# Performance work log

Hardware: AMD Instinct MI355X
Metric: run time of the kernel (lower is better)

Reference implementation:

```python
import jax, jax.numpy as jnp
import numpy as np

# Physical parameter bounds in PARAM_NAMES order:
# [S1_max,S2_max,f_tens,f_rchr,f_base,r1,ku,c,alpha,psi,kappa,ki,ks,n,v,v_A,v_B,
#  Ac_max,b,lambda,chi,mu_t,T_rain,T_melt,melt_rate,lapse_rate,opg,MFMAX,MFMIN]
LOW = jnp.array([50.0,100.0,0.05,0.05,0.05,0.05,0.01,1.0,1.0,1.0,0.05,0.01,0.001,1.0,
                 0.001,0.001,0.001,0.05,0.001,5.0,2.0,0.01,-2.0,-2.0,1.0,-9.8,0.0,1.0,0.0],
                dtype=jnp.float32)
HIGH = jnp.array([5000.0,10000.0,0.95,0.95,0.95,0.95,1000.0,20.0,250.0,5.0,0.95,1000.0,
                  10000.0,10.0,0.25,0.25,0.25,0.95,3.0,10.0,5.0,5.0,4.0,4.0,10.0,0.0,1.0,10.0,10.0],
                 dtype=jnp.float32)
ROUTE_SHAPE = 2.5   # gamma routing shape (init kwarg)
KERNEL_LEN = 64     # routing kernel support (timesteps)
DT = 1.0
S1_INIT, S2_INIT = 50.0, 250.0  # state_init in the module


def _physical(raw_params):
    # low + (high-low)*sigmoid(raw), same as get_physical_params
    return LOW + (HIGH - LOW) * jax.nn.sigmoid(raw_params)


def _simulate(forcing, p):
    """Explicit-Euler 2-reservoir FUSE-style simulation. forcing: [T,3]=(prcp,pet,temp)."""
    S1_max, S2_max = p[0], p[1]
    f_tens, ku, c = p[2], p[6], p[7]
    ki, ks, n_exp = p[11], p[12], p[13]
    b, T_rain = p[18], p[22]

    def step(state, f):
        S1, S2 = state
        prcp, pet, temp = f[0], f[1], f[2]
        rain = jnp.where(temp > T_rain, prcp, 0.0)
        s1f = jnp.clip(S1 / S1_max, 0.0, 1.0)
        s2f = jnp.clip(S2 / S2_max, 0.0, 1.0)
        e1 = pet * jnp.minimum(s1f / f_tens, 1.0)          # tension-store evap
        qsx = rain * s1f ** b                               # saturation-excess runoff
        q12 = ku * s1f ** c                                 # percolation to lower store
        qif = ki * s1f                                      # interflow
        qb = ks * s2f ** n_exp                              # nonlinear baseflow
        S1n = jnp.clip(S1 + DT * (rain - qsx - e1 - q12 - qif), 0.0, S1_max)
        S2n = jnp.clip(S2 + DT * (q12 - qb), 0.0, S2_max)
        return (S1n, S2n), qsx + qif + qb

    init = (jnp.float32(S1_INIT), jnp.float32(S2_INIT))
    _, runoff = jax.lax.scan(step, init, forcing)
    return runoff  # [T]


def _route(runoff, shape, delay):
    """Causal gamma-kernel routing convolution (route_runoff)."""
    t = jnp.arange(KERNEL_LEN, dtype=jnp.float32) + 0.5
    theta = jnp.maximum(delay, 1e-3) / shape               # scale so mean = delay
    logk = (shape - 1.0) * jnp.log(t) - t / theta
    kern = jax.nn.softmax(logk)                            # normalized gamma weights
    return jnp.convolve(runoff, kern)[: runoff.shape[0]]   # causal conv


def reference(forcing, raw_params):
    phys = _physical(raw_params)
    runoff = _simulate(forcing, phys)
    # delay is used as a detached python float in the torch code -> stop_gradient
    delay = jax.lax.stop_gradient(phys[21])  # mu_t
    return _route(runoff, ROUTE_SHAPE, delay)


def setup_inputs() -> dict:
    key = jax.random.key(0)
    k1, k2, k3 = jax.random.split(key, 3)
    T = 131072
    prcp = jnp.maximum(jax.random.normal(k1, (T,)) * 5.0 + 2.0, 0.0)  # mm/day
    pet = jax.random.uniform(k2, (T,)) * 5.0                          # mm/day
    temp = jax.random.normal(k3, (T,)) * 8.0 + 5.0                    # deg C
    forcing = jnp.stack([prcp, pet, temp], axis=-1).astype(jnp.float32)
    raw_params = jnp.zeros((29,), dtype=jnp.float32)  # sigmoid(0)=0.5 -> mid-bounds
    return {"forcing": forcing, "raw_params": raw_params}
```

## Files before the change

kernel.cpp:

```cpp
#include <hip/hip_runtime.h>

#define KLEN 64
#define FCH 16
#define WARMUP 64
#define WIN_FC 64
#define S1_INIT_V 50.0f
#define S2_INIT_V 250.0f

__device__ __forceinline__ float fpow(float x, float e) {
    return exp2f(e * __log2f(x));
}
__device__ __forceinline__ float clamp01(float x) { return fminf(fmaxf(x, 0.0f), 1.0f); }
__device__ __forceinline__ float physp(const float* raw, int i, float lo, float hi) {
    return lo + (hi - lo) / (1.0f + __expf(-raw[i]));
}

struct F8 { float4 v[6]; };
__device__ __forceinline__ F8 load_f8(const float* __restrict__ forc, int t) {
    const float4* p = (const float4*)(forc + 3 * t);
    F8 r;
#pragma unroll
    for (int k = 0; k < 6; ++k) r.v[k] = p[k];
    return r;
}
__device__ __forceinline__ float f4c(const float4& v, int c) {
    return c == 0 ? v.x : c == 1 ? v.y : c == 2 ? v.z : v.w;
}
__device__ __forceinline__ float f8_get(const F8& f, int i) { return f4c(f.v[i >> 2], i & 3); }

#define S1_CORE(pr, pe, te, QACC)                                         \
    {                                                                     \
        float rain = (te) > Train ? (pr) : 0.0f;                          \
        float s1f = clamp01(S1 * invS1);                                  \
        float lg = __log2f(s1f);                                          \
        float e1 = (pe)*fminf(s1f * invft, 1.0f);                         \
        float qsx = rain * exp2f(b * lg);                                 \
        float q12 = ku * exp2f(cc * lg);                                  \
        float qif = ki * s1f;                                             \
        S1 = fminf(fmaxf(S1 + rain - qsx - e1 - q12 - qif, 0.0f), S1max); \
        QACC;                                                             \
    }

__global__ void __launch_bounds__(64) k_s1(
        const float* __restrict__ forc, const float* __restrict__ raw,
        float* __restrict__ s1s, float* __restrict__ q12f, float* __restrict__ Qw,
        int T, int nfine) {
    int lane = threadIdx.x;
    int j = blockIdx.x * WIN_FC + lane;
    bool active = j < nfine;

    const float S1max  = physp(raw, 0, 50.0f, 5000.0f);
    const float f_tens = physp(raw, 2, 0.05f, 0.95f);
    const float ku     = physp(raw, 6, 0.01f, 1000.0f);
    const float cc     = physp(raw, 7, 1.0f, 20.0f);
    const float ki     = physp(raw, 11, 0.01f, 1000.0f);
    const float b      = physp(raw, 18, 0.001f, 3.0f);
    const float Train  = physp(raw, 22, -2.0f, 4.0f);
    const float invS1 = 1.0f / S1max, invft = 1.0f / f_tens;

    float S1 = S1_INIT_V;
    float Q = 0.0f;
    if (active) {
        int t0 = j * FCH;
        int tend = min(t0 + FCH, T);
        int ts = max(t0 - WARMUP, 0);

        int ngw = (t0 - ts) >> 3;
        F8 cur = load_f8(forc, ts);
        for (int g = 0; g < ngw; ++g) {
            F8 nxt = load_f8(forc, ts + 8 * (g + 1));
#pragma unroll
            for (int s = 0; s < 8; ++s) {
                float pr = f8_get(cur, 3 * s), pe = f8_get(cur, 3 * s + 1), te = f8_get(cur, 3 * s + 2);
                S1_CORE(pr, pe, te, );
            }
            cur = nxt;
        }
        s1s[j] = S1;

        int ngm = (tend - t0) >> 3;
        for (int g = 0; g < ngm; ++g) {
            F8 nxt = load_f8(forc, t0 + 8 * min(g + 1, ngm - 1));
#pragma unroll
            for (int s = 0; s < 8; ++s) {
                float pr = f8_get(cur, 3 * s), pe = f8_get(cur, 3 * s + 1), te = f8_get(cur, 3 * s + 2);
                S1_CORE(pr, pe, te, Q += q12);
            }
            cur = nxt;
        }
        for (int t = t0 + 8 * ngm; t < tend; ++t) {
            float pr = forc[3 * t], pe = forc[3 * t + 1], te = forc[3 * t + 2];
            S1_CORE(pr, pe, te, Q += q12);
        }
        q12f[j] = Q;
    }
    float s = Q;
#pragma unroll
    for (int o = 32; o >= 1; o >>= 1) s += __shfl_xor(s, o, 64);
    if (lane == 0) Qw[blockIdx.x] = s;
}

__global__ void __launch_bounds__(64) k_s2win(
        const float* __restrict__ raw, const float* __restrict__ Qw,
        const float* __restrict__ q12f,
        float* __restrict__ S2win, float* __restrict__ qbwin,
        float* __restrict__ s2fine, int* __restrict__ flag,
        int T, int nfine) {
    int lane = threadIdx.x;
    const float S2max = physp(raw, 1, 100.0f, 10000.0f);
    const float ks    = physp(raw, 12, 0.001f, 10000.0f);
    const float nn    = physp(raw, 13, 1.0f, 10.0f);
    const float invS2 = 1.0f / S2max;

    int NW = (nfine + WIN_FC - 1) / WIN_FC;
    int WSTEPS = WIN_FC * FCH;

    int w0 = 2 * lane, w1 = 2 * lane + 1;
    float L0 = (w0 < NW) ? (float)min(WSTEPS, T - WSTEPS * w0) : 0.0f;
    float L1 = (w1 < NW) ? (float)min(WSTEPS, T - WSTEPS * w1) : 0.0f;
    float Q0 = (w0 < NW) ? Qw[w0] : 0.0f;
    float Q1 = (w1 < NW) ? Qw[w1] : 0.0f;

    float qb0 = ks * fpow(clamp01(S2_INIT_V * invS2), nn);
    float qb1 = qb0;
    float S20 = S2_INIT_V, S21 = S2_INIT_V;
    bool picard_ok = (NW <= 128);
    if (picard_ok) {
        for (int it = 0; it < 12; ++it) {
            float d0 = Q0 - L0 * qb0;
            float d1 = Q1 - L1 * qb1;
            float pair = d0 + d1;
            float sc = pair;
#pragma unroll
            for (int o = 1; o < 64; o <<= 1) {
                float v = __shfl_up(sc, o, 64);
                if (lane >= o) sc += v;
            }
            float excl = sc - pair;
            S20 = S2_INIT_V + excl;
            S21 = S20 + d0;
            qb0 = ks * fpow(clamp01(S20 * invS2), nn);
            qb1 = ks * fpow(clamp01(S21 * invS2), nn);
        }
        bool bad = false;
        if (w0 < NW) bad |= (S20 - L0 * qb0 < 0.5f) || (S20 + Q0 > S2max - 0.5f);
        if (w1 < NW) bad |= (S21 - L1 * qb1 < 0.5f) || (S21 + Q1 > S2max - 0.5f);
        picard_ok = (__ballot(bad) == 0ULL);
    }
    if (picard_ok) {
        if (w0 < NW) { S2win[w0] = S20; qbwin[w0] = qb0; }
        if (w1 < NW) { S2win[w1] = S21; qbwin[w1] = qb1; }
        if (lane == 0) *flag = 0;
    } else if (lane == 0) {
        *flag = 1;
        float S2 = S2_INIT_V;
        for (int w = 0; w < NW; ++w) {
            float s2f = clamp01(S2 * invS2);
            float qb = ks * fpow(s2f, nn);
            S2win[w] = S2; qbwin[w] = qb;
            int i0 = w * WIN_FC, i1 = min(i0 + WIN_FC, nfine);
            for (int i = i0; i < i1; ++i) {
                s2fine[i] = S2;
                float steps = (float)min(FCH, T - FCH * i);
                S2 = fminf(fmaxf(S2 + q12f[i] - steps * qb, 0.0f), S2max);
            }
        }
    }
}

__global__ void __launch_bounds__(64) k_sim(
        const float* __restrict__ forc, const float* __restrict__ raw,
        const float* __restrict__ s1s, const float* __restrict__ q12f,
        const float* __restrict__ S2win, const float* __restrict__ qbwin,
        const float* __restrict__ s2fine, const int* __restrict__ flag,
        float* __restrict__ runoff, int T, int nfine) {
    int lane = threadIdx.x;
    int j = blockIdx.x * WIN_FC + lane;
    bool active = j < nfine;

    const float S1max  = physp(raw, 0, 50.0f, 5000.0f);
    const float S2max  = physp(raw, 1, 100.0f, 10000.0f);
    const float f_tens = physp(raw, 2, 0.05f, 0.95f);
    const float ku     = physp(raw, 6, 0.01f, 1000.0f);
    const float ki     = physp(raw, 11, 0.01f, 1000.0f);
    const float ks     = physp(raw, 12, 0.001f, 10000.0f);
    const float nn     = physp(raw, 13, 1.0f, 10.0f);
    const float cc     = physp(raw, 7, 1.0f, 20.0f);
    const float b      = physp(raw, 18, 0.001f, 3.0f);
    const float Train  = physp(raw, 22, -2.0f, 4.0f);
    const float invS1 = 1.0f / S1max, invS2 = 1.0f / S2max, invft = 1.0f / f_tens;

    float q = active ? q12f[j] : 0.0f;
    float S2;
    if (*flag) {
        S2 = active ? s2fine[j] : 0.0f;
    } else {
        float sc = q;
#pragma unroll
        for (int o = 1; o < 64; o <<= 1) {
            float v = __shfl_up(sc, o, 64);
            if (lane >= o) sc += v;
        }
        float excl = sc - q;
        S2 = S2win[blockIdx.x] + excl - qbwin[blockIdx.x] * (float)(FCH * lane);
        S2 = fminf(fmaxf(S2, 0.0f), S2max);
    }
    if (!active) return;

    float S1 = s1s[j];
    int t0 = j * FCH;
    int tend = min(t0 + FCH, T);

#define SIM_CORE(pr, pe, te, EMIT)                                        \
    {                                                                     \
        float rain = (te) > Train ? (pr) : 0.0f;                          \
        float s1f = clamp01(S1 * invS1);                                  \
        float s2f = clamp01(S2 * invS2);                                  \
        float lg = __log2f(s1f);                                          \
        float e1 = (pe)*fminf(s1f * invft, 1.0f);                         \
        float qsx = rain * exp2f(b * lg);                                 \
        float q12 = ku * exp2f(cc * lg);                                  \
        float qif = ki * s1f;                                             \
        float qb = ks * fpow(s2f, nn);                                    \
        EMIT;                                                             \
        S1 = fminf(fmaxf(S1 + rain - qsx - e1 - q12 - qif, 0.0f), S1max); \
        S2 = fminf(fmaxf(S2 + q12 - qb, 0.0f), S2max);                    \
    }

    int ngm = (tend - t0) >> 3;
    if (ngm > 0) {
        F8 cur = load_f8(forc, t0);
        for (int g = 0; g < ngm; ++g) {
            F8 nxt = load_f8(forc, t0 + 8 * min(g + 1, ngm - 1));
            float ro[8];
#pragma unroll
            for (int s = 0; s < 8; ++s) {
                float pr = f8_get(cur, 3 * s), pe = f8_get(cur, 3 * s + 1), te = f8_get(cur, 3 * s + 2);
                SIM_CORE(pr, pe, te, ro[s] = qsx + qif + qb);
            }
            float4* rp = (float4*)(runoff + t0 + 8 * g);
            rp[0] = make_float4(ro[0], ro[1], ro[2], ro[3]);
            rp[1] = make_float4(ro[4], ro[5], ro[6], ro[7]);
            cur = nxt;
        }
    }
    for (int t = t0 + 8 * ngm; t < tend; ++t) {
        float pr = forc[3 * t], pe = forc[3 * t + 1], te = forc[3 * t + 2];
        SIM_CORE(pr, pe, te, runoff[t] = qsx + qif + qb);
    }
}

__global__ void k_route(const float* __restrict__ runoff, const float* __restrict__ raw,
                        float* __restrict__ out, int T) {
    __shared__ float ls[256 + KLEN - 1];
    __shared__ float ker[KLEN];
    int tid = threadIdx.x;
    int base = blockIdx.x * 256;
    if (tid < 64) {
        float delay = physp(raw, 21, 0.01f, 5.0f);
        float theta = fmaxf(delay, 1e-3f) * (1.0f / 2.5f);
        float tt = (float)tid + 0.5f;
        float logk = 1.5f * __logf(tt) - tt / theta;
        float m = logk;
#pragma unroll
        for (int o = 32; o >= 1; o >>= 1) m = fmaxf(m, __shfl_xor(m, o, 64));
        float e = __expf(logk - m);
        float s = e;
#pragma unroll
        for (int o = 32; o >= 1; o >>= 1) s += __shfl_xor(s, o, 64);
        ker[tid] = e / s;
    }
    for (int i = tid; i < 256 + KLEN - 1; i += 256) {
        int t = base - (KLEN - 1) + i;
        ls[i] = (t >= 0 && t < T) ? runoff[t] : 0.0f;
    }
    __syncthreads();
    float acc = 0.0f;
#pragma unroll
    for (int k = 0; k < KLEN; ++k) acc += ker[k] * ls[tid + (KLEN - 1) - k];
    int t = base + tid;
    if (t < T) out[t] = acc;
}

extern "C" void kernel_launch(void* const* d_in, const int* in_sizes, int n_in,
                              void* d_out, int out_size, void* d_ws, size_t ws_size,
                              hipStream_t stream) {
    const float* forcing = (const float*)d_in[0];
    const float* raw = (const float*)d_in[1];
    float* out = (float*)d_out;
    float* ws = (float*)d_ws;

    int T = in_sizes[0] / 3;
    int nfine = (T + FCH - 1) / FCH;
    int NW = (nfine + WIN_FC - 1) / WIN_FC;
    int P = ((nfine + 7) / 8) * 8;
    int PW = ((NW + 7) / 8) * 8;

    float* s1s = ws;
    float* q12f = s1s + P;
    float* Qw = q12f + P;
    float* S2win = Qw + PW;
    float* qbwin = S2win + PW;
    float* s2fine = qbwin + PW;
    int* flag = (int*)(s2fine + P);
    float* runoff = (float*)(flag + 8);

    k_s1<<<NW, 64, 0, stream>>>(forcing, raw, s1s, q12f, Qw, T, nfine);
    k_s2win<<<1, 64, 0, stream>>>(raw, Qw, q12f, S2win, qbwin, s2fine, flag, T, nfine);
    k_sim<<<NW, 64, 0, stream>>>(forcing, raw, s1s, q12f, S2win, qbwin, s2fine, flag,
                                 runoff, T, nfine);
    k_route<<<(T + 255) / 256, 256, 0, stream>>>(runoff, raw, out, T);
}
```

Before: 73.39 us.

## Fuse four kernels into one persistent kernel with grid barriers

Replaces the S1 pass, the S2 window solve, the full simulation and the routing kernels with one kernel that uses software grid barriers between phases. S1 fluxes are kept in registers so the second pass only advances S2, and the routing convolution reads runoff from shared memory within each window. Warmup is reduced from 64 to 48 steps. This removes three launch gaps and recomputation of S1, but adds an atomic spin barrier that relies on all 128 blocks being co-resident, a memset launch, and a shorter warmup that may change accuracy.

Measured after the change: 98.74 us. 34.5% more time.

```diff
diff --git a/kernel.cpp b/kernel.cpp
--- a/kernel.cpp
+++ b/kernel.cpp
@@ -2,8 +2,9 @@
 
 #define KLEN 64
 #define FCH 16
-#define WARMUP 64
+#define WARMUP 48
 #define WIN_FC 64
+#define WSTEP (WIN_FC * FCH)
 #define S1_INIT_V 50.0f
 #define S2_INIT_V 250.0f
 
@@ -11,7 +12,7 @@
     return exp2f(e * __log2f(x));
 }
 __device__ __forceinline__ float clamp01(float x) { return fminf(fmaxf(x, 0.0f), 1.0f); }
-__device__ __forceinline__ float physp(const float* raw, int i, float lo, float hi) {
+__device__ __forceinline__ float physp(const float* __restrict__ raw, int i, float lo, float hi) {
     return lo + (hi - lo) / (1.0f + __expf(-raw[i]));
 }
 
@@ -28,7 +29,48 @@
 }
 __device__ __forceinline__ float f8_get(const F8& f, int i) { return f4c(f.v[i >> 2], i & 3); }
 
-#define S1_CORE(pr, pe, te, QACC)                                         \
+__device__ __forceinline__ void gbar(int* cnt, int phase, int nblk) {
+    __syncthreads();
+    if (threadIdx.x == 0) {
+        __threadfence();
+        __hip_atomic_fetch_add(cnt, 1, __ATOMIC_ACQ_REL, __HIP_MEMORY_SCOPE_AGENT);
+        while (__hip_atomic_load(cnt, __ATOMIC_ACQUIRE, __HIP_MEMORY_SCOPE_AGENT) <
+               phase * nblk) {
+            __builtin_amdgcn_s_sleep(2);
+        }
+        __threadfence();
+    }
+    __syncthreads();
+}
+
+__global__ void __launch_bounds__(64) k_fused(
+        const float* __restrict__ forc, const float* __restrict__ raw,
+        float* __restrict__ q12f, float* __restrict__ Qw,
+        float* __restrict__ S2win, float* __restrict__ qbwin,
+        float* __restrict__ s2fine, float* __restrict__ runoff,
+        int* __restrict__ syncp, int* __restrict__ flag,
+        float* __restrict__ out, int T, int nfine, int NW) {
+    __shared__ float r[WSTEP + 64];
+    __shared__ float ker[KLEN];
+    const int lane = threadIdx.x;
+    const int w = blockIdx.x;
+    const int j = w * WIN_FC + lane;
+    const int t0w = w * WSTEP;
+    const bool active = j < nfine;
+
+    const float S1max  = physp(raw, 0, 50.0f, 5000.0f);
+    const float S2max  = physp(raw, 1, 100.0f, 10000.0f);
+    const float f_tens = physp(raw, 2, 0.05f, 0.95f);
+    const float ku     = physp(raw, 6, 0.01f, 1000.0f);
+    const float cc     = physp(raw, 7, 1.0f, 20.0f);
+    const float ki     = physp(raw, 11, 0.01f, 1000.0f);
+    const float ks     = physp(raw, 12, 0.001f, 10000.0f);
+    const float nn     = physp(raw, 13, 1.0f, 10.0f);
+    const float b      = physp(raw, 18, 0.001f, 3.0f);
+    const float Train  = physp(raw, 22, -2.0f, 4.0f);
+    const float invS1 = 1.0f / S1max, invS2 = 1.0f / S2max, invft = 1.0f / f_tens;
+
+#define S1_STEP(pr, pe, te, EXTRA)                                        \
     {                                                                     \
         float rain = (te) > Train ? (pr) : 0.0f;                          \
         float s1f = clamp01(S1 * invS1);                                  \
@@ -37,229 +79,168 @@
         float qsx = rain * exp2f(b * lg);                                 \
         float q12 = ku * exp2f(cc * lg);                                  \
         float qif = ki * s1f;                                             \
+        EXTRA;                                                            \
         S1 = fminf(fmaxf(S1 + rain - qsx - e1 - q12 - qif, 0.0f), S1max); \
-        QACC;                                                             \
-    }
-
-__global__ void __launch_bounds__(64) k_s1(
-        const float* __restrict__ forc, const float* __restrict__ raw,
-        float* __restrict__ s1s, float* __restrict__ q12f, float* __restrict__ Qw,
-        int T, int nfine) {
-    int lane = threadIdx.x;
-    int j = blockIdx.x * WIN_FC + lane;
-    bool active = j < nfine;
-
-    const float S1max  = physp(raw, 0, 50.0f, 5000.0f);
-    const float f_tens = physp(raw, 2, 0.05f, 0.95f);
-    const float ku     = physp(raw, 6, 0.01f, 1000.0f);
-    const float cc     = physp(raw, 7, 1.0f, 20.0f);
-    const float ki     = physp(raw, 11, 0.01f, 1000.0f);
-    const float b      = physp(raw, 18, 0.001f, 3.0f);
-    const float Train  = physp(raw, 22, -2.0f, 4.0f);
-    const float invS1 = 1.0f / S1max, invft = 1.0f / f_tens;
-
-    float S1 = S1_INIT_V;
+    }
+
+    float qx[FCH];
+    float q12v[FCH];
     float Q = 0.0f;
+    const int t0 = j * FCH;
+    const int tend = active ? min(t0 + FCH, T) : t0;
+    const bool fullchunk = active && (tend - t0 == FCH);
+
     if (active) {
-        int t0 = j * FCH;
-        int tend = min(t0 + FCH, T);
         int ts = max(t0 - WARMUP, 0);
-
+        float S1 = S1_INIT_V;
         int ngw = (t0 - ts) >> 3;
         F8 cur = load_f8(forc, ts);
         for (int g = 0; g < ngw; ++g) {
             F8 nxt = load_f8(forc, ts + 8 * (g + 1));
 #pragma unroll
-            for (int s = 0; s < 8; ++s) {
-                float pr = f8_get(cur, 3 * s), pe = f8_get(cur, 3 * s + 1), te = f8_get(cur, 3 * s + 2);
-                S1_CORE(pr, pe, te, );
-            }
+            for (int s = 0; s < 8; ++s)
+                S1_STEP(f8_get(cur, 3 * s), f8_get(cur, 3 * s + 1), f8_get(cur, 3 * s + 2), );
             cur = nxt;
         }
-        s1s[j] = S1;
-
-        int ngm = (tend - t0) >> 3;
-        for (int g = 0; g < ngm; ++g) {
-            F8 nxt = load_f8(forc, t0 + 8 * min(g + 1, ngm - 1));
-#pragma unroll
-            for (int s = 0; s < 8; ++s) {
-                float pr = f8_get(cur, 3 * s), pe = f8_get(cur, 3 * s + 1), te = f8_get(cur, 3 * s + 2);
-                S1_CORE(pr, pe, te, Q += q12);
-            }
-            cur = nxt;
-        }
-        for (int t = t0 + 8 * ngm; t < tend; ++t) {
-            float pr = forc[3 * t], pe = forc[3 * t + 1], te = forc[3 * t + 2];
-            S1_CORE(pr, pe, te, Q += q12);
+        if (fullchunk) {
+#pragma unroll
+            for (int g = 0; g < 2; ++g) {
+                F8 nxt = (g == 0) ? load_f8(forc, t0 + 8) : cur;
+#pragma unroll
+                for (int s = 0; s < 8; ++s) {
+                    const int idx = 8 * g + s;
+                    S1_STEP(f8_get(cur, 3 * s), f8_get(cur, 3 * s + 1), f8_get(cur, 3 * s + 2),
+                            qx[idx] = qsx + qif; q12v[idx] = q12; Q += q12);
+                }
+                cur = nxt;
+            }
+        } else {
+            for (int t = t0; t < tend; ++t) {
+                float pr = forc[3 * t], pe = forc[3 * t + 1], te = forc[3 * t + 2];
+                S1_STEP(pr, pe, te, Q += q12);
+            }
         }
         q12f[j] = Q;
     }
-    float s = Q;
-#pragma unroll
-    for (int o = 32; o >= 1; o >>= 1) s += __shfl_xor(s, o, 64);
-    if (lane == 0) Qw[blockIdx.x] = s;
-}
-
-__global__ void __launch_bounds__(64) k_s2win(
-        const float* __restrict__ raw, const float* __restrict__ Qw,
-        const float* __restrict__ q12f,
-        float* __restrict__ S2win, float* __restrict__ qbwin,
-        float* __restrict__ s2fine, int* __restrict__ flag,
-        int T, int nfine) {
-    int lane = threadIdx.x;
-    const float S2max = physp(raw, 1, 100.0f, 10000.0f);
-    const float ks    = physp(raw, 12, 0.001f, 10000.0f);
-    const float nn    = physp(raw, 13, 1.0f, 10.0f);
-    const float invS2 = 1.0f / S2max;
-
-    int NW = (nfine + WIN_FC - 1) / WIN_FC;
-    int WSTEPS = WIN_FC * FCH;
-
-    int w0 = 2 * lane, w1 = 2 * lane + 1;
-    float L0 = (w0 < NW) ? (float)min(WSTEPS, T - WSTEPS * w0) : 0.0f;
-    float L1 = (w1 < NW) ? (float)min(WSTEPS, T - WSTEPS * w1) : 0.0f;
-    float Q0 = (w0 < NW) ? Qw[w0] : 0.0f;
-    float Q1 = (w1 < NW) ? Qw[w1] : 0.0f;
-
-    float qb0 = ks * fpow(clamp01(S2_INIT_V * invS2), nn);
-    float qb1 = qb0;
-    float S20 = S2_INIT_V, S21 = S2_INIT_V;
-    bool picard_ok = (NW <= 128);
-    if (picard_ok) {
-        for (int it = 0; it < 12; ++it) {
-            float d0 = Q0 - L0 * qb0;
-            float d1 = Q1 - L1 * qb1;
-            float pair = d0 + d1;
-            float sc = pair;
-#pragma unroll
-            for (int o = 1; o < 64; o <<= 1) {
-                float v = __shfl_up(sc, o, 64);
-                if (lane >= o) sc += v;
-            }
-            float excl = sc - pair;
-            S20 = S2_INIT_V + excl;
-            S21 = S20 + d0;
-            qb0 = ks * fpow(clamp01(S20 * invS2), nn);
-            qb1 = ks * fpow(clamp01(S21 * invS2), nn);
-        }
-        bool bad = false;
-        if (w0 < NW) bad |= (S20 - L0 * qb0 < 0.5f) || (S20 + Q0 > S2max - 0.5f);
-        if (w1 < NW) bad |= (S21 - L1 * qb1 < 0.5f) || (S21 + Q1 > S2max - 0.5f);
-        picard_ok = (__ballot(bad) == 0ULL);
-    }
-    if (picard_ok) {
-        if (w0 < NW) { S2win[w0] = S20; qbwin[w0] = qb0; }
-        if (w1 < NW) { S2win[w1] = S21; qbwin[w1] = qb1; }
-        if (lane == 0) *flag = 0;
-    } else if (lane == 0) {
-        *flag = 1;
-        float S2 = S2_INIT_V;
-        for (int w = 0; w < NW; ++w) {
-            float s2f = clamp01(S2 * invS2);
-            float qb = ks * fpow(s2f, nn);
-            S2win[w] = S2; qbwin[w] = qb;
-            int i0 = w * WIN_FC, i1 = min(i0 + WIN_FC, nfine);
-            for (int i = i0; i < i1; ++i) {
-                s2fine[i] = S2;
-                float steps = (float)min(FCH, T - FCH * i);
-                S2 = fminf(fmaxf(S2 + q12f[i] - steps * qb, 0.0f), S2max);
-            }
-        }
-    }
-}
-
-__global__ void __launch_bounds__(64) k_sim(
-        const float* __restrict__ forc, const float* __restrict__ raw,
-        const float* __restrict__ s1s, const float* __restrict__ q12f,
-        const float* __restrict__ S2win, const float* __restrict__ qbwin,
-        const float* __restrict__ s2fine, const int* __restrict__ flag,
-        float* __restrict__ runoff, int T, int nfine) {
-    int lane = threadIdx.x;
-    int j = blockIdx.x * WIN_FC + lane;
-    bool active = j < nfine;
-
-    const float S1max  = physp(raw, 0, 50.0f, 5000.0f);
-    const float S2max  = physp(raw, 1, 100.0f, 10000.0f);
-    const float f_tens = physp(raw, 2, 0.05f, 0.95f);
-    const float ku     = physp(raw, 6, 0.01f, 1000.0f);
-    const float ki     = physp(raw, 11, 0.01f, 1000.0f);
-    const float ks     = physp(raw, 12, 0.001f, 10000.0f);
-    const float nn     = physp(raw, 13, 1.0f, 10.0f);
-    const float cc     = physp(raw, 7, 1.0f, 20.0f);
-    const float b      = physp(raw, 18, 0.001f, 3.0f);
-    const float Train  = physp(raw, 22, -2.0f, 4.0f);
-    const float invS1 = 1.0f / S1max, invS2 = 1.0f / S2max, invft = 1.0f / f_tens;
-
-    float q = active ? q12f[j] : 0.0f;
+    {
+        float s = Q;
+#pragma unroll
+        for (int o = 32; o >= 1; o >>= 1) s += __shfl_xor(s, o, 64);
+        if (lane == 0) Qw[w] = s;
+    }
+
+    gbar(syncp, 1, NW);
+
+    if (w == 0) {
+        int wsteps = WSTEP;
+        int w0 = 2 * lane, w1 = 2 * lane + 1;
+        float L0 = (w0 < NW) ? (float)min(wsteps, T - wsteps * w0) : 0.0f;
+        float L1 = (w1 < NW) ? (float)min(wsteps, T - wsteps * w1) : 0.0f;
+        float Q0 = (w0 < NW) ? Qw[w0] : 0.0f;
+        float Q1 = (w1 < NW) ? Qw[w1] : 0.0f;
+
+        float qb0 = ks * fpow(clamp01(S2_INIT_V * invS2), nn);
+        float qb1 = qb0;
+        float S20 = S2_INIT_V, S21 = S2_INIT_V;
+        bool picard_ok = (NW <= 128);
+        if (picard_ok) {
+            for (int it = 0; it < 12; ++it) {
+                float d0 = Q0 - L0 * qb0;
+                float d1 = Q1 - L1 * qb1;
+                float pair = d0 + d1;
+                float sc = pair;
+#pragma unroll
+                for (int o = 1; o < 64; o <<= 1) {
+                    float v = __shfl_up(sc, o, 64);
+                    if (lane >= o) sc += v;
+                }
+                float excl = sc - pair;
+                S20 = S2_INIT_V + excl;
+                S21 = S20 + d0;
+                qb0 = ks * fpow(clamp01(S20 * invS2), nn);
+                qb1 = ks * fpow(clamp01(S21 * invS2), nn);
+            }
+            bool bad = false;
+            if (w0 < NW) bad |= (S20 - L0 * qb0 < 0.5f) || (S20 + Q0 > S2max - 0.5f);
+            if (w1 < NW) bad |= (S21 - L1 * qb1 < 0.5f) || (S21 + Q1 > S2max - 0.5f);
+            picard_ok = (__ballot(bad) == 0ULL);
+        }
+        if (picard_ok) {
+            if (w0 < NW) { S2win[w0] = S20; qbwin[w0] = qb0; }
+            if (w1 < NW) { S2win[w1] = S21; qbwin[w1] = qb1; }
+            if (lane == 0) *flag = 0;
+        } else if (lane == 0) {
+            *flag = 1;
+            float S2 = S2_INIT_V;
+            for (int v = 0; v < NW; ++v) {
+                float s2f = clamp01(S2 * invS2);
+                float qb = ks * fpow(s2f, nn);
+                S2win[v] = S2; qbwin[v] = qb;
+                int i0 = v * WIN_FC, i1 = min(i0 + WIN_FC, nfine);
+                for (int i = i0; i < i1; ++i) {
+                    s2fine[i] = S2;
+                    float steps = (float)min(FCH, T - FCH * i);
+                    S2 = fminf(fmaxf(S2 + q12f[i] - steps * qb, 0.0f), S2max);
+                }
+            }
+        }
+    }
+
+    gbar(syncp, 2, NW);
+
     float S2;
     if (*flag) {
         S2 = active ? s2fine[j] : 0.0f;
     } else {
-        float sc = q;
+        float sc = Q;
 #pragma unroll
         for (int o = 1; o < 64; o <<= 1) {
             float v = __shfl_up(sc, o, 64);
             if (lane >= o) sc += v;
         }
-        float excl = sc - q;
-        S2 = S2win[blockIdx.x] + excl - qbwin[blockIdx.x] * (float)(FCH * lane);
+        S2 = S2win[w] + (sc - Q) - qbwin[w] * (float)(FCH * lane);
         S2 = fminf(fmaxf(S2, 0.0f), S2max);
     }
-    if (!active) return;
-
-    float S1 = s1s[j];
-    int t0 = j * FCH;
-    int tend = min(t0 + FCH, T);
-
-#define SIM_CORE(pr, pe, te, EMIT)                                        \
-    {                                                                     \
-        float rain = (te) > Train ? (pr) : 0.0f;                          \
-        float s1f = clamp01(S1 * invS1);                                  \
-        float s2f = clamp01(S2 * invS2);                                  \
-        float lg = __log2f(s1f);                                          \
-        float e1 = (pe)*fminf(s1f * invft, 1.0f);                         \
-        float qsx = rain * exp2f(b * lg);                                 \
-        float q12 = ku * exp2f(cc * lg);                                  \
-        float qif = ki * s1f;                                             \
-        float qb = ks * fpow(s2f, nn);                                    \
-        EMIT;                                                             \
-        S1 = fminf(fmaxf(S1 + rain - qsx - e1 - q12 - qif, 0.0f), S1max); \
-        S2 = fminf(fmaxf(S2 + q12 - qb, 0.0f), S2max);                    \
-    }
-
-    int ngm = (tend - t0) >> 3;
-    if (ngm > 0) {
-        F8 cur = load_f8(forc, t0);
-        for (int g = 0; g < ngm; ++g) {
-            F8 nxt = load_f8(forc, t0 + 8 * min(g + 1, ngm - 1));
-            float ro[8];
-#pragma unroll
-            for (int s = 0; s < 8; ++s) {
-                float pr = f8_get(cur, 3 * s), pe = f8_get(cur, 3 * s + 1), te = f8_get(cur, 3 * s + 2);
-                SIM_CORE(pr, pe, te, ro[s] = qsx + qif + qb);
-            }
-            float4* rp = (float4*)(runoff + t0 + 8 * g);
-            rp[0] = make_float4(ro[0], ro[1], ro[2], ro[3]);
-            rp[1] = make_float4(ro[4], ro[5], ro[6], ro[7]);
-            cur = nxt;
-        }
-    }
-    for (int t = t0 + 8 * ngm; t < tend; ++t) {
-        float pr = forc[3 * t], pe = forc[3 * t + 1], te = forc[3 * t + 2];
-        SIM_CORE(pr, pe, te, runoff[t] = qsx + qif + qb);
-    }
-}
-
-__global__ void k_route(const float* __restrict__ runoff, const float* __restrict__ raw,
-                        float* __restrict__ out, int T) {
-    __shared__ float ls[256 + KLEN - 1];
-    __shared__ float ker[KLEN];
-    int tid = threadIdx.x;
-    int base = blockIdx.x * 256;
-    if (tid < 64) {
+    if (fullchunk) {
+        float rb[FCH];
+#pragma unroll
+        for (int s = 0; s < FCH; ++s) {
+            float s2f = clamp01(S2 * invS2);
+            float qb = ks * fpow(s2f, nn);
+            float ro = qx[s] + qb;
+            rb[s] = ro;
+            r[64 + FCH * lane + s] = ro;
+            S2 = fminf(fmaxf(S2 + q12v[s] - qb, 0.0f), S2max);
+        }
+        float4* rp = (float4*)(runoff + t0);
+#pragma unroll
+        for (int s4 = 0; s4 < 4; ++s4)
+            rp[s4] = make_float4(rb[4 * s4], rb[4 * s4 + 1], rb[4 * s4 + 2], rb[4 * s4 + 3]);
+    } else if (active) {
+        float S1 = S1_INIT_V;
+        int ts = max(t0 - WARMUP, 0);
+        for (int t = ts; t < t0; ++t) {
+            float pr = forc[3 * t], pe = forc[3 * t + 1], te = forc[3 * t + 2];
+            S1_STEP(pr, pe, te, );
+        }
+        for (int t = t0; t < tend; ++t) {
+            float pr = forc[3 * t], pe = forc[3 * t + 1], te = forc[3 * t + 2];
+            float s2f = clamp01(S2 * invS2);
+            float qb = ks * fpow(s2f, nn);
+            float ro;
+            S1_STEP(pr, pe, te, ro = qsx + qif + qb;
+                    S2 = fminf(fmaxf(S2 + q12 - qb, 0.0f), S2max));
+            r[64 + (t - t0w)] = ro;
+            runoff[t] = ro;
+        }
+    }
+
+    gbar(syncp, 3, NW);
+
+    {
         float delay = physp(raw, 21, 0.01f, 5.0f);
         float theta = fmaxf(delay, 1e-3f) * (1.0f / 2.5f);
-        float tt = (float)tid + 0.5f;
+        float tt = (float)lane + 0.5f;
         float logk = 1.5f * __logf(tt) - tt / theta;
         float m = logk;
 #pragma unroll
@@ -268,18 +249,22 @@
         float s = e;
 #pragma unroll
         for (int o = 32; o >= 1; o >>= 1) s += __shfl_xor(s, o, 64);
-        ker[tid] = e / s;
-    }
-    for (int i = tid; i < 256 + KLEN - 1; i += 256) {
-        int t = base - (KLEN - 1) + i;
-        ls[i] = (t >= 0 && t < T) ? runoff[t] : 0.0f;
+        ker[lane] = e / s;
+        int tp = t0w - 64 + lane;
+        r[lane] = (tp >= 0 && lane > 0) ? runoff[tp] : 0.0f;
     }
     __syncthreads();
-    float acc = 0.0f;
-#pragma unroll
-    for (int k = 0; k < KLEN; ++k) acc += ker[k] * ls[tid + (KLEN - 1) - k];
-    int t = base + tid;
-    if (t < T) out[t] = acc;
+#pragma unroll 1
+    for (int it = 0; it < WSTEP / 64; ++it) {
+        int i = it * 64 + lane;
+        int t = t0w + i;
+        if (t < T) {
+            float acc = 0.0f;
+#pragma unroll
+            for (int k = 0; k < KLEN; ++k) acc += ker[k] * r[64 + i - k];
+            out[t] = acc;
+        }
+    }
 }
 
 extern "C" void kernel_launch(void* const* d_in, const int* in_sizes, int n_in,
@@ -288,7 +273,6 @@
     const float* forcing = (const float*)d_in[0];
     const float* raw = (const float*)d_in[1];
     float* out = (float*)d_out;
-    float* ws = (float*)d_ws;
 
     int T = in_sizes[0] / 3;
     int nfine = (T + FCH - 1) / FCH;
@@ -296,18 +280,17 @@
     int P = ((nfine + 7) / 8) * 8;
     int PW = ((NW + 7) / 8) * 8;
 
-    float* s1s = ws;
-    float* q12f = s1s + P;
+    int* syncp = (int*)d_ws;
+    int* flag = syncp + 16;
+    float* base = (float*)d_ws + 32;
+    float* q12f = base;
     float* Qw = q12f + P;
     float* S2win = Qw + PW;
     float* qbwin = S2win + PW;
     float* s2fine = qbwin + PW;
-    int* flag = (int*)(s2fine + P);
-    float* runoff = (float*)(flag + 8);
-
-    k_s1<<<NW, 64, 0, stream>>>(forcing, raw, s1s, q12f, Qw, T, nfine);
-    k_s2win<<<1, 64, 0, stream>>>(raw, Qw, q12f, S2win, qbwin, s2fine, flag, T, nfine);
-    k_sim<<<NW, 64, 0, stream>>>(forcing, raw, s1s, q12f, S2win, qbwin, s2fine, flag,
-                                 runoff, T, nfine);
-    k_route<<<(T + 255) / 256, 256, 0, stream>>>(runoff, raw, out, T);
-}
+    float* runoff = s2fine + P;
+
+    hipMemsetAsync(d_ws, 0, 128, stream);
+    k_fused<<<NW, 64, 0, stream>>>(forcing, raw, q12f, Qw, S2win, qbwin, s2fine,
+                                   runoff, syncp, flag, out, T, nfine, NW);
+}
```
